# Optimization experiments

Measured on AMD Instinct MI355X. Metric: run time of the kernel, lower is better.

## Reference

```python
import jax, jax.numpy as jnp
import numpy as np

A_CONST = 0.1
B_CONST = 0.2
C_CONST = 0.8

INPUT_SIZE = 1024
HIDDEN_SIZE = 2048
BATCH = 32768
SIGMA = 0.02


def acti_func(x, a, b, c):
    # piecewise: a*(1 - x/b) for x<=b ; 0 for b<x<c ; a*(x-c)/(1-c) for x>=c
    low = -a * x / b + a
    high = a * x / (1.0 - c) + a * c / (c - 1.0)
    return jnp.where(x <= b, low, jnp.where(x >= c, high, jnp.zeros_like(x)))


def setup_inputs() -> dict:
    key = jax.random.key(0)
    ks = jax.random.split(key, 4)
    x = jax.random.normal(ks[0], (BATCH, INPUT_SIZE), dtype=jnp.float32)
    W0 = jax.random.normal(ks[1], (INPUT_SIZE, HIDDEN_SIZE), dtype=jnp.float32) * SIGMA
    b0 = jnp.zeros((HIDDEN_SIZE,), dtype=jnp.float32)
    W1 = jax.random.normal(ks[2], (HIDDEN_SIZE, HIDDEN_SIZE), dtype=jnp.float32) * SIGMA
    b1 = jnp.zeros((HIDDEN_SIZE,), dtype=jnp.float32)
    W2 = jax.random.normal(ks[3], (HIDDEN_SIZE, 1), dtype=jnp.float32) * SIGMA
    b2 = jnp.zeros((1,), dtype=jnp.float32)
    return {"x": x, "W0": W0, "b0": b0, "W1": W1, "b1": b1, "W2": W2, "b2": b2}


def reference(x, W0, b0, W1, b1, W2, b2):
    h = jax.nn.elu(x @ W0 + b0)
    h = jax.nn.elu(h @ W1 + b1)
    out = jax.nn.sigmoid(h @ W2 + b2)  # [B, 1]
    alpha = acti_func(out, A_CONST, B_CONST, C_CONST)
    return out, alpha
```

## Files before the change

kernel.cpp:

```cpp
#include <hip/hip_runtime.h>
#include <hip/hip_bf16.h>
#include <stdint.h>

typedef unsigned short u16;
typedef __bf16 bf16x8 __attribute__((ext_vector_type(8)));
typedef float floatx4 __attribute__((ext_vector_type(4)));

__device__ __forceinline__ u16 f2bf(float f) {
  union { float f; unsigned u; } c; c.f = f;
  unsigned r = c.u + 0x7fffu + ((c.u >> 16) & 1u);
  return (u16)(r >> 16);
}

__device__ __forceinline__ void load_lds16(const void* g, void* l) {
  __builtin_amdgcn_global_load_lds(
      (const __attribute__((address_space(1))) void*)g,
      (__attribute__((address_space(3))) void*)l,
      16, 0, 0);
}

__global__ __launch_bounds__(256) void preamble(
    const float* __restrict__ x, const float* __restrict__ W0,
    const float* __restrict__ W1,
    u16* __restrict__ Xb, u16* __restrict__ Wt0, u16* __restrict__ Wt1,
    float* __restrict__ z)
{
  __shared__ float tile[32][33];
  const int bid = blockIdx.x;
  const int t = threadIdx.x;

  if (bid < 32768) {
    int i = bid * 256 + t;
    float4 f = ((const float4*)x)[i];
    ushort4 u;
    u.x = f2bf(f.x); u.y = f2bf(f.y); u.z = f2bf(f.z); u.w = f2bf(f.w);
    ((ushort4*)Xb)[i] = u;
  } else if (bid < 32768 + 2048) {
    int tb = bid - 32768;
    int bx = (tb & 63) * 32, by = (tb >> 6) * 32;
    int tx = t & 31, ty = t >> 5;
    #pragma unroll
    for (int i = 0; i < 32; i += 8)
      tile[ty + i][tx] = W0[(size_t)(by + ty + i) * 2048 + bx + tx];
    __syncthreads();
    #pragma unroll
    for (int i = 0; i < 32; i += 8)
      Wt0[(size_t)(bx + ty + i) * 1024 + by + tx] = f2bf(tile[tx][ty + i]);
  } else if (bid < 32768 + 2048 + 4096) {
    int tb = bid - (32768 + 2048);
    int bx = (tb & 63) * 32, by = (tb >> 6) * 32;
    int tx = t & 31, ty = t >> 5;
    #pragma unroll
    for (int i = 0; i < 32; i += 8)
      tile[ty + i][tx] = W1[(size_t)(by + ty + i) * 2048 + bx + tx];
    __syncthreads();
    #pragma unroll
    for (int i = 0; i < 32; i += 8)
      Wt1[(size_t)(bx + ty + i) * 2048 + by + tx] = f2bf(tile[tx][ty + i]);
  } else {
    int tb = bid - (32768 + 2048 + 4096);
    ((float4*)z)[tb * 256 + t] = (float4){0.f, 0.f, 0.f, 0.f};
  }
}

template<bool FUSE_HEAD>
__global__ __launch_bounds__(256) void gemm_bt_fused(
    const u16* __restrict__ A,
    const u16* __restrict__ Bt,
    const float* __restrict__ bias,
    u16* __restrict__ C,
    const float* __restrict__ W2,
    float* __restrict__ z,
    int M, int N, int K)
{
  __shared__ u16 As[128 * 64];
  __shared__ u16 Bs[128 * 64];

  const int t = threadIdx.x;
  const int w = t >> 6;
  const int l = t & 63;
  const int wm = w >> 1;
  const int wn = w & 1;
  const int lm = l & 15;
  const int q  = l >> 4;

  const int n0 = blockIdx.x * 128;
  const int m0 = blockIdx.y * 128;

  floatx4 acc[4][4];
  #pragma unroll
  for (int i = 0; i < 4; ++i)
    #pragma unroll
    for (int j = 0; j < 4; ++j)
      acc[i][j] = (floatx4){0.f, 0.f, 0.f, 0.f};

  const int rowoff = t >> 3;
  const int lc8 = ((t & 7) ^ (rowoff & 7)) * 8;
  const u16* Ap[4];
  const u16* Bp[4];
  #pragma unroll
  for (int k = 0; k < 4; ++k) {
    Ap[k] = A  + (size_t)(m0 + k * 32 + rowoff) * K + lc8;
    Bp[k] = Bt + (size_t)(n0 + k * 32 + rowoff) * K + lc8;
  }
  const int ldsoff = t * 8;

  const int sw0 = ((0 * 4 + q) ^ (lm & 7)) * 8;
  const int sw1 = ((1 * 4 + q) ^ (lm & 7)) * 8;

  for (int k0 = 0; k0 < K; k0 += 64) {
    __syncthreads();
    #pragma unroll
    for (int k = 0; k < 4; ++k) {
      load_lds16(Ap[k] + k0, &As[k * 2048 + ldsoff]);
      load_lds16(Bp[k] + k0, &Bs[k * 2048 + ldsoff]);
    }
    __syncthreads();

    {
      bf16x8 af[4], bfr[4];
      #pragma unroll
      for (int i = 0; i < 4; ++i)
        af[i] = *(const bf16x8*)(As + (wm * 64 + i * 16 + lm) * 64 + sw0);
      #pragma unroll
      for (int j = 0; j < 4; ++j)
        bfr[j] = *(const bf16x8*)(Bs + (wn * 64 + j * 16 + lm) * 64 + sw0);
      #pragma unroll
      for (int i = 0; i < 4; ++i)
        #pragma unroll
        for (int j = 0; j < 4; ++j)
          acc[i][j] = __builtin_amdgcn_mfma_f32_16x16x32_bf16(af[i], bfr[j], acc[i][j], 0, 0, 0);
    }
    {
      bf16x8 af[4], bfr[4];
      #pragma unroll
      for (int i = 0; i < 4; ++i)
        af[i] = *(const bf16x8*)(As + (wm * 64 + i * 16 + lm) * 64 + sw1);
      #pragma unroll
      for (int j = 0; j < 4; ++j)
        bfr[j] = *(const bf16x8*)(Bs + (wn * 64 + j * 16 + lm) * 64 + sw1);
      #pragma unroll
      for (int i = 0; i < 4; ++i)
        #pragma unroll
        for (int j = 0; j < 4; ++j)
          acc[i][j] = __builtin_amdgcn_mfma_f32_16x16x32_bf16(af[i], bfr[j], acc[i][j], 0, 0, 0);
    }
  }

  float bv[4];
  #pragma unroll
  for (int j = 0; j < 4; ++j) bv[j] = bias[n0 + wn * 64 + j * 16 + lm];

  if (!FUSE_HEAD) {
    #pragma unroll
    for (int i = 0; i < 4; ++i) {
      #pragma unroll
      for (int r = 0; r < 4; ++r) {
        int grow = m0 + wm * 64 + i * 16 + q * 4 + r;
        size_t base = (size_t)grow * N + n0 + wn * 64 + lm;
        #pragma unroll
        for (int j = 0; j < 4; ++j) {
          float v = acc[i][j][r] + bv[j];
          v = v > 0.f ? v : (__expf(v) - 1.f);
          C[base + j * 16] = f2bf(v);
        }
      }
    }
  } else {
    float w2v[4];
    #pragma unroll
    for (int j = 0; j < 4; ++j) w2v[j] = W2[n0 + wn * 64 + j * 16 + lm];
    #pragma unroll
    for (int i = 0; i < 4; ++i) {
      #pragma unroll
      for (int r = 0; r < 4; ++r) {
        float p = 0.f;
        #pragma unroll
        for (int j = 0; j < 4; ++j) {
          float v = acc[i][j][r] + bv[j];
          v = v > 0.f ? v : (__expf(v) - 1.f);
          p += v * w2v[j];
        }
        p += __shfl_xor(p, 1);
        p += __shfl_xor(p, 2);
        p += __shfl_xor(p, 4);
        p += __shfl_xor(p, 8);
        if (lm == 0) atomicAdd(&z[m0 + wm * 64 + i * 16 + q * 4 + r], p);
      }
    }
  }
}

__global__ __launch_bounds__(256) void sigmoid_alpha(
    const float* __restrict__ z, const float* __restrict__ b2,
    float* __restrict__ out, int B)
{
  int i = blockIdx.x * blockDim.x + threadIdx.x;
  if (i >= B) return;
  float o = 1.f / (1.f + expf(-(z[i] + b2[0])));
  float alpha;
  if (o <= 0.2f)      alpha = 0.1f - 0.5f * o;
  else if (o >= 0.8f) alpha = 0.5f * o - 0.4f;
  else                alpha = 0.f;
  out[i] = o;
  out[B + i] = alpha;
}

extern "C" void kernel_launch(void* const* d_in, const int* in_sizes, int n_in,
                              void* d_out, int out_size, void* d_ws, size_t ws_size,
                              hipStream_t stream) {
  const int BATCH = 32768, IN = 1024, HID = 2048;

  const float* x  = (const float*)d_in[0];
  const float* W0 = (const float*)d_in[1];
  const float* b0 = (const float*)d_in[2];
  const float* W1 = (const float*)d_in[3];
  const float* b1 = (const float*)d_in[4];
  const float* W2 = (const float*)d_in[5];
  const float* b2 = (const float*)d_in[6];
  float* out = (float*)d_out;

  char* ws = (char*)d_ws;
  u16* Xb   = (u16*)(ws);
  u16* Wt0  = (u16*)(ws + (size_t)67108864);
  u16* Wt1  = (u16*)(ws + (size_t)71303168);
  u16* h0   = (u16*)(ws + (size_t)79691776);
  float* z  = (float*)(ws + (size_t)213909504);

  preamble<<<32768 + 2048 + 4096 + 32, 256, 0, stream>>>(x, W0, W1, Xb, Wt0, Wt1, z);
  gemm_bt_fused<false><<<dim3(HID / 128, BATCH / 128), 256, 0, stream>>>(
      Xb, Wt0, b0, h0, nullptr, nullptr, BATCH, HID, IN);
  gemm_bt_fused<true><<<dim3(HID / 128, BATCH / 128), 256, 0, stream>>>(
      h0, Wt1, b1, nullptr, W2, z, BATCH, HID, HID);
  sigmoid_alpha<<<BATCH / 256, 256, 0, stream>>>(z, b2, out, BATCH);
}
```

Before: 683.2 us.

## Rewrite GEMMs as 256x256 tiles with 8 waves and double-buffered LDS pipeline

Replaces the 128x128, 4-wave GEMM with a 256x256 tile computed by 8 waves. LDS is double-buffered (128 KB) and global-to-LDS prefetch runs two k-steps ahead, interleaved with MFMA phases under s_setprio and manual vmcnt waits. Workgroup IDs are remapped for better L2 locality. The larger tile raises data reuse per load and hides memory latency behind compute, at the cost of high register and LDS pressure (only one workgroup per CU can fit) and fragile hand-written synchronization.

```diff
diff --git a/kernel.cpp b/kernel.cpp
--- a/kernel.cpp
+++ b/kernel.cpp
@@ -17,6 +17,13 @@
       (const __attribute__((address_space(1))) void*)g,
       (__attribute__((address_space(3))) void*)l,
       16, 0, 0);
+}
+
+__device__ __forceinline__ void memclob() { asm volatile("" ::: "memory"); }
+__device__ __forceinline__ void barrier_() {
+  memclob();
+  __builtin_amdgcn_s_barrier();
+  memclob();
 }
 
 __global__ __launch_bounds__(256) void preamble(
@@ -64,7 +71,7 @@
 }
 
 template<bool FUSE_HEAD>
-__global__ __launch_bounds__(256) void gemm_bt_fused(
+__global__ __launch_bounds__(512, 2) void gemm256_8p(
     const u16* __restrict__ A,
     const u16* __restrict__ Bt,
     const float* __restrict__ bias,
@@ -73,78 +80,141 @@
     float* __restrict__ z,
     int M, int N, int K)
 {
-  __shared__ u16 As[128 * 64];
-  __shared__ u16 Bs[128 * 64];
+  __shared__ u16 lds[65536];
 
   const int t = threadIdx.x;
+  const int l = t & 63;
   const int w = t >> 6;
-  const int l = t & 63;
-  const int wm = w >> 1;
-  const int wn = w & 1;
+  const int wm = w >> 2;
+  const int wn = w & 3;
   const int lm = l & 15;
   const int q  = l >> 4;
 
-  const int n0 = blockIdx.x * 128;
-  const int m0 = blockIdx.y * 128;
-
-  floatx4 acc[4][4];
+  const int nwg = gridDim.x;
+  int wg = blockIdx.x;
+  wg = (wg & 7) * (nwg >> 3) + (wg >> 3);
+  const int nbn = N >> 8;
+  const int n0 = (wg % nbn) << 8;
+  const int m0 = (wg / nbn) << 8;
+
+  const int rowoff = t >> 3;
+  const int lc8 = ((t & 7) ^ (rowoff & 7)) * 8;
+  const u16* ApA0 = A + (size_t)(m0 + rowoff) * K + lc8;
+  const u16* ApA1 = A + (size_t)(m0 + 128 + rowoff) * K + lc8;
+  const int bq = rowoff >> 5;
+  const int br = rowoff & 31;
+  const u16* BpB0 = Bt + (size_t)(n0 + bq * 64 + br) * K + lc8;
+  const u16* BpB1 = Bt + (size_t)(n0 + (2 + bq) * 64 + br) * K + lc8;
+  const int ldst = t * 8;
+
+#define SLOT(p, idx) (((p) * 4 + (idx)) * 8192)
+
+  auto stage_a = [&](int p, int s, int kt) {
+    load_lds16(ApA0 + (size_t)s * 64 * K + (size_t)kt * 64, &lds[SLOT(p, s) + ldst]);
+    load_lds16(ApA1 + (size_t)s * 64 * K + (size_t)kt * 64, &lds[SLOT(p, s) + 4096 + ldst]);
+  };
+  auto stage_b = [&](int p, int s, int kt) {
+    load_lds16(BpB0 + (size_t)s * 32 * K + (size_t)kt * 64, &lds[SLOT(p, 2 + s) + ldst]);
+    load_lds16(BpB1 + (size_t)s * 32 * K + (size_t)kt * 64, &lds[SLOT(p, 2 + s) + 4096 + ldst]);
+  };
+
+  const int ck0 = ((0 * 4 + q) ^ (lm & 7)) * 8;
+  const int ck1 = ((1 * 4 + q) ^ (lm & 7)) * 8;
+  const int arow = (wm * 64 + lm) * 64;
+  const int brow = (wn * 32 + lm) * 64;
+#define RDA(p, i, ck) (*(const bf16x8*)&lds[SLOT(p, (i) >> 2) + arow + ((i) & 3) * 1024 + (ck)])
+#define RDB(p, j, ck) (*(const bf16x8*)&lds[SLOT(p, 2 + ((j) >> 1)) + brow + ((j) & 1) * 1024 + (ck)])
+#define MFMA(d, x, y) d = __builtin_amdgcn_mfma_f32_16x16x32_bf16(x, y, d, 0, 0, 0)
+
+  floatx4 acc[8][4];
   #pragma unroll
-  for (int i = 0; i < 4; ++i)
+  for (int i = 0; i < 8; ++i)
     #pragma unroll
     for (int j = 0; j < 4; ++j)
       acc[i][j] = (floatx4){0.f, 0.f, 0.f, 0.f};
 
-  const int rowoff = t >> 3;
-  const int lc8 = ((t & 7) ^ (rowoff & 7)) * 8;
-  const u16* Ap[4];
-  const u16* Bp[4];
-  #pragma unroll
-  for (int k = 0; k < 4; ++k) {
-    Ap[k] = A  + (size_t)(m0 + k * 32 + rowoff) * K + lc8;
-    Bp[k] = Bt + (size_t)(n0 + k * 32 + rowoff) * K + lc8;
-  }
-  const int ldsoff = t * 8;
-
-  const int sw0 = ((0 * 4 + q) ^ (lm & 7)) * 8;
-  const int sw1 = ((1 * 4 + q) ^ (lm & 7)) * 8;
-
-  for (int k0 = 0; k0 < K; k0 += 64) {
-    __syncthreads();
-    #pragma unroll
-    for (int k = 0; k < 4; ++k) {
-      load_lds16(Ap[k] + k0, &As[k * 2048 + ldsoff]);
-      load_lds16(Bp[k] + k0, &Bs[k * 2048 + ldsoff]);
+  bf16x8 a[8][2];
+  bf16x8 b[2][2];
+
+  const int NK = K >> 6;
+
+  stage_a(0, 0, 0); memclob(); stage_a(0, 1, 0); memclob();
+  stage_b(0, 0, 0); memclob(); stage_b(0, 1, 0); memclob();
+  stage_a(1, 0, 1); memclob(); stage_a(1, 1, 1); memclob();
+  stage_b(1, 0, 1);
+  asm volatile("s_waitcnt vmcnt(6)" ::: "memory");
+  barrier_();
+
+  #pragma unroll 2
+  for (int g = 0; g < NK; ++g) {
+    const int p = g & 1;
+    const bool s1 = (g + 1 < NK);
+    const bool s2 = (g + 2 < NK);
+
+    #pragma unroll
+    for (int i = 0; i < 4; ++i) { a[i][0] = RDA(p, i, ck0); a[i][1] = RDA(p, i, ck1); }
+    #pragma unroll
+    for (int j = 0; j < 2; ++j) { b[j][0] = RDB(p, j, ck0); b[j][1] = RDB(p, j, ck1); }
+    if (s1) stage_b(p ^ 1, 1, g + 1);
+    barrier_();
+    __builtin_amdgcn_s_setprio(1);
+    #pragma unroll
+    for (int i = 0; i < 4; ++i)
+      #pragma unroll
+      for (int j = 0; j < 2; ++j) {
+        MFMA(acc[i][j], a[i][0], b[j][0]);
+        MFMA(acc[i][j], a[i][1], b[j][1]);
+      }
+    __builtin_amdgcn_s_setprio(0);
+    barrier_();
+
+    #pragma unroll
+    for (int i = 4; i < 8; ++i) { a[i][0] = RDA(p, i, ck0); a[i][1] = RDA(p, i, ck1); }
+    if (s2) stage_a(p, 0, g + 2);
+    barrier_();
+    __builtin_amdgcn_s_setprio(1);
+    #pragma unroll
+    for (int i = 4; i < 8; ++i)
+      #pragma unroll
+      for (int j = 0; j < 2; ++j) {
+        MFMA(acc[i][j], a[i][0], b[j][0]);
+        MFMA(acc[i][j], a[i][1], b[j][1]);
+      }
+    __builtin_amdgcn_s_setprio(0);
+    barrier_();
+
+    #pragma unroll
+    for (int j = 0; j < 2; ++j) { b[j][0] = RDB(p, 2 + j, ck0); b[j][1] = RDB(p, 2 + j, ck1); }
+    if (s2) stage_a(p, 1, g + 2);
+    barrier_();
+    __builtin_amdgcn_s_setprio(1);
+    #pragma unroll
+    for (int i = 0; i < 4; ++i)
+      #pragma unroll
+      for (int j = 0; j < 2; ++j) {
+        MFMA(acc[i][2 + j], a[i][0], b[j][0]);
+        MFMA(acc[i][2 + j], a[i][1], b[j][1]);
+      }
+    __builtin_amdgcn_s_setprio(0);
+    barrier_();
+
+    if (s2) {
+      stage_b(p, 0, g + 2);
+      asm volatile("s_waitcnt vmcnt(6)" ::: "memory");
+    } else if (s1) {
+      asm volatile("s_waitcnt vmcnt(0)" ::: "memory");
     }
-    __syncthreads();
-
-    {
-      bf16x8 af[4], bfr[4];
-      #pragma unroll
-      for (int i = 0; i < 4; ++i)
-        af[i] = *(const bf16x8*)(As + (wm * 64 + i * 16 + lm) * 64 + sw0);
-      #pragma unroll
-      for (int j = 0; j < 4; ++j)
-        bfr[j] = *(const bf16x8*)(Bs + (wn * 64 + j * 16 + lm) * 64 + sw0);
-      #pragma unroll
-      for (int i = 0; i < 4; ++i)
-        #pragma unroll
-        for (int j = 0; j < 4; ++j)
-          acc[i][j] = __builtin_amdgcn_mfma_f32_16x16x32_bf16(af[i], bfr[j], acc[i][j], 0, 0, 0);
-    }
-    {
-      bf16x8 af[4], bfr[4];
-      #pragma unroll
-      for (int i = 0; i < 4; ++i)
-        af[i] = *(const bf16x8*)(As + (wm * 64 + i * 16 + lm) * 64 + sw1);
-      #pragma unroll
-      for (int j = 0; j < 4; ++j)
-        bfr[j] = *(const bf16x8*)(Bs + (wn * 64 + j * 16 + lm) * 64 + sw1);
-      #pragma unroll
-      for (int i = 0; i < 4; ++i)
-        #pragma unroll
-        for (int j = 0; j < 4; ++j)
-          acc[i][j] = __builtin_amdgcn_mfma_f32_16x16x32_bf16(af[i], bfr[j], acc[i][j], 0, 0, 0);
-    }
+    barrier_();
+    __builtin_amdgcn_s_setprio(1);
+    #pragma unroll
+    for (int i = 4; i < 8; ++i)
+      #pragma unroll
+      for (int j = 0; j < 2; ++j) {
+        MFMA(acc[i][2 + j], a[i][0], b[j][0]);
+        MFMA(acc[i][2 + j], a[i][1], b[j][1]);
+      }
+    __builtin_amdgcn_s_setprio(0);
+    barrier_();
   }
 
   float bv[4];
@@ -153,10 +223,10 @@
 
   if (!FUSE_HEAD) {
     #pragma unroll
-    for (int i = 0; i < 4; ++i) {
+    for (int i = 0; i < 8; ++i) {
       #pragma unroll
       for (int r = 0; r < 4; ++r) {
-        int grow = m0 + wm * 64 + i * 16 + q * 4 + r;
+        int grow = m0 + wm * 128 + i * 16 + q * 4 + r;
         size_t base = (size_t)grow * N + n0 + wn * 64 + lm;
         #pragma unroll
         for (int j = 0; j < 4; ++j) {
@@ -171,24 +241,28 @@
     #pragma unroll
     for (int j = 0; j < 4; ++j) w2v[j] = W2[n0 + wn * 64 + j * 16 + lm];
     #pragma unroll
-    for (int i = 0; i < 4; ++i) {
+    for (int i = 0; i < 8; ++i) {
       #pragma unroll
       for (int r = 0; r < 4; ++r) {
-        float p = 0.f;
+        float pacc = 0.f;
         #pragma unroll
         for (int j = 0; j < 4; ++j) {
           float v = acc[i][j][r] + bv[j];
           v = v > 0.f ? v : (__expf(v) - 1.f);
-          p += v * w2v[j];
+          pacc += v * w2v[j];
         }
-        p += __shfl_xor(p, 1);
-        p += __shfl_xor(p, 2);
-        p += __shfl_xor(p, 4);
-        p += __shfl_xor(p, 8);
-        if (lm == 0) atomicAdd(&z[m0 + wm * 64 + i * 16 + q * 4 + r], p);
+        pacc += __shfl_xor(pacc, 1);
+        pacc += __shfl_xor(pacc, 2);
+        pacc += __shfl_xor(pacc, 4);
+        pacc += __shfl_xor(pacc, 8);
+        if (lm == 0) atomicAdd(&z[m0 + wm * 128 + i * 16 + q * 4 + r], pacc);
       }
     }
   }
+#undef SLOT
+#undef RDA
+#undef RDB
+#undef MFMA
 }
 
 __global__ __launch_bounds__(256) void sigmoid_alpha(
@@ -227,10 +301,12 @@
   u16* h0   = (u16*)(ws + (size_t)79691776);
   float* z  = (float*)(ws + (size_t)213909504);
 
+  const int grid = (BATCH / 256) * (HID / 256);
+
   preamble<<<32768 + 2048 + 4096 + 32, 256, 0, stream>>>(x, W0, W1, Xb, Wt0, Wt1, z);
-  gemm_bt_fused<false><<<dim3(HID / 128, BATCH / 128), 256, 0, stream>>>(
+  gemm256_8p<false><<<grid, 512, 0, stream>>>(
       Xb, Wt0, b0, h0, nullptr, nullptr, BATCH, HID, IN);
-  gemm_bt_fused<true><<<dim3(HID / 128, BATCH / 128), 256, 0, stream>>>(
+  gemm256_8p<true><<<grid, 512, 0, stream>>>(
       h0, Wt1, b1, nullptr, W2, z, BATCH, HID, HID);
   sigmoid_alpha<<<BATCH / 256, 256, 0, stream>>>(z, b2, out, BATCH);
 }
```

Result: faster. 623.0 us (-8.8%).
